# Optimization experiments

Hardware: AMD Instinct MI355X
Metric: run time of the kernel (lower is better)

Reference implementation:

```python
import jax, jax.numpy as jnp
import numpy as np

CH = 512
GROUPS = 32
EPS = 1e-6


def setup_inputs() -> dict:
    key = jax.random.key(0)
    ks = jax.random.split(key, 12)
    b, c, h, w = 4, CH, 64, 64
    std = 1.0 / np.sqrt(c)
    return {
        "x": jax.random.normal(ks[0], (b, c, h, w), dtype=jnp.float32),
        "norm_gamma": jnp.ones((c,), jnp.float32),
        "norm_beta": jnp.zeros((c,), jnp.float32),
        "wq": jax.random.normal(ks[1], (c, c), jnp.float32) * std,
        "bq": jax.random.normal(ks[2], (c,), jnp.float32) * 0.01,
        "wk": jax.random.normal(ks[3], (c, c), jnp.float32) * std,
        "bk": jax.random.normal(ks[4], (c,), jnp.float32) * 0.01,
        "wv": jax.random.normal(ks[5], (c, c), jnp.float32) * std,
        "bv": jax.random.normal(ks[6], (c,), jnp.float32) * 0.01,
        "wo": jax.random.normal(ks[7], (c, c), jnp.float32) * std,
        "bo": jax.random.normal(ks[8], (c,), jnp.float32) * 0.01,
    }


def _group_norm(x, gamma, beta):
    b, c, h, w = x.shape
    xg = x.reshape(b, GROUPS, c // GROUPS, h, w)
    mean = xg.mean(axis=(2, 3, 4), keepdims=True)
    var = xg.var(axis=(2, 3, 4), keepdims=True)
    xn = ((xg - mean) * jax.lax.rsqrt(var + EPS)).reshape(b, c, h, w)
    return xn * gamma[None, :, None, None] + beta[None, :, None, None]


def reference(x, norm_gamma, norm_beta, wq, bq, wk, bk, wv, bv, wo, bo):
    b, c, h, w = x.shape
    hn = _group_norm(x, norm_gamma, norm_beta)
    hs = hn.reshape(b, c, h * w)  # [b, c, n]
    # 1x1 convs == per-pixel matmuls over channel dim (weight[out,in])
    q = jnp.einsum('oc,bcn->bno', wq, hs) + bq  # [b, n, c]
    k = jnp.einsum('oc,bcn->bon', wk, hs) + bk[None, :, None]  # [b, c, n]
    v = jnp.einsum('oc,bcn->bno', wv, hs) + bv  # [b, n, c]
    scale = c ** (-0.5)
    attn = jax.nn.softmax(jnp.einsum('bnc,bcm->bnm', q, k) * scale, axis=-1)
    out = jnp.einsum('bnm,bmc->bnc', attn, v)  # [b, n, c]
    out = jnp.einsum('oc,bnc->bon', wo, out) + bo[None, :, None]  # [b, c, n]
    return x + out.reshape(b, c, h, w)
```

## Files before the change

kernel.cpp:

```cpp
#include <hip/hip_runtime.h>
#include <hip/hip_bf16.h>
#include <cstdint>

typedef __bf16 bf16;
typedef __bf16 bf16x8 __attribute__((ext_vector_type(8)));
typedef __bf16 bf16x4 __attribute__((ext_vector_type(4)));
typedef float f32x4 __attribute__((ext_vector_type(4)));

__device__ __forceinline__ void gld_lds16(const void* g, void* l) {
  __builtin_amdgcn_global_load_lds((const __attribute__((address_space(1))) void*)g,
                                   (__attribute__((address_space(3))) void*)l, 16, 0, 0);
}

enum { BIAS_NONE = 0, BIAS_COL = 1, BIAS_ROW = 2 };
enum { OUT_BF16 = 0, OUT_F32_RESID = 1 };

template<int BIAS_MODE, int OUT_MODE>
__global__ __launch_bounds__(256)
void gemm_bt(const bf16* __restrict__ A, long sA, int lda,
             const bf16* __restrict__ Bm, long sB, int ldb,
             void* __restrict__ Cv, long sC, int ldc,
             const float* __restrict__ bias,
             const float* __restrict__ resid, long sR,
             int K, float scale)
{
  const int bm = blockIdx.x, bn = blockIdx.y, bz = blockIdx.z;
  const char* Ab = (const char*)(A + (long)bz * sA);
  const char* Bb = (const char*)(Bm + (long)bz * sB);
  const int tid = threadIdx.x;
  const int wave = tid >> 6, lane = tid & 63;
  const int wr = wave >> 1, wc = wave & 1;

  __shared__ __attribute__((aligned(128))) char lds[32768];
  char* ldsA = lds;
  char* ldsB = lds + 16384;

  uint32_t aoff[4], boff[4];
#pragma unroll
  for (int i = 0; i < 4; ++i) {
    uint32_t ra = (uint32_t)(wr * 64 + i * 16 + (lane & 15));
    uint32_t la = ra * 128u + (uint32_t)((lane >> 4) << 4);
    aoff[i] = la ^ ((la >> 3) & 0x70u);
    uint32_t rb = (uint32_t)(wc * 64 + i * 16 + (lane & 15));
    uint32_t lb = rb * 128u + (uint32_t)((lane >> 4) << 4);
    boff[i] = lb ^ ((lb >> 3) & 0x70u);
  }

  uint32_t srow[4], sinb[4];
#pragma unroll
  for (int t = 0; t < 4; ++t) {
    uint32_t paddr = (uint32_t)(((wave * 4 + t) * 64 + lane) * 16);
    uint32_t laddr = paddr ^ ((paddr >> 3) & 0x70u);
    srow[t] = laddr >> 7;
    sinb[t] = laddr & 127u;
  }

  const long ldab = (long)lda * 2, ldbb = (long)ldb * 2;
  const long arow0 = (long)bm * 128, brow0 = (long)bn * 128;

  f32x4 acc[4][4] = {};

  const int nK = K >> 6;
  for (int kt = 0; kt < nK; ++kt) {
    const long k0b = (long)kt * 128;
#pragma unroll
    for (int t = 0; t < 4; ++t) {
      gld_lds16(Ab + (arow0 + srow[t]) * ldab + k0b + sinb[t],
                ldsA + (wave * 4 + t) * 1024);
      gld_lds16(Bb + (brow0 + srow[t]) * ldbb + k0b + sinb[t],
                ldsB + (wave * 4 + t) * 1024);
    }
    __syncthreads();
#pragma unroll
    for (int kk = 0; kk < 2; ++kk) {
      bf16x8 af[4], bfr[4];
#pragma unroll
      for (int i = 0; i < 4; ++i) {
        af[i]  = *(const bf16x8*)(ldsA + (aoff[i] ^ (kk << 6)));
        bfr[i] = *(const bf16x8*)(ldsB + (boff[i] ^ (kk << 6)));
      }
#pragma unroll
      for (int mi = 0; mi < 4; ++mi)
#pragma unroll
        for (int ni = 0; ni < 4; ++ni)
          acc[mi][ni] = __builtin_amdgcn_mfma_f32_16x16x32_bf16(af[mi], bfr[ni], acc[mi][ni], 0, 0, 0);
    }
    __syncthreads();
  }

  const int cl = lane & 15, rq = lane >> 4;
  const long row0 = (long)bm * 128 + wr * 64;
  const long col0 = (long)bn * 128 + wc * 64;

  if constexpr (OUT_MODE == OUT_BF16) {
    bf16* Co = (bf16*)Cv + (long)bz * sC;
#pragma unroll
    for (int mi = 0; mi < 4; ++mi) {
#pragma unroll
      for (int ni = 0; ni < 4; ++ni) {
        const long col = col0 + ni * 16 + cl;
        float bc = 0.f;
        if (BIAS_MODE == BIAS_COL) bc = bias[col];
#pragma unroll
        for (int j = 0; j < 4; ++j) {
          const long row = row0 + mi * 16 + rq * 4 + j;
          float v = acc[mi][ni][j] * scale + bc;
          if (BIAS_MODE == BIAS_ROW) v += bias[row];
          Co[row * ldc + col] = (bf16)v;
        }
      }
    }
  } else {
    float* Co = (float*)Cv + (long)bz * sC;
    const float* X = resid + (long)bz * sR;
#pragma unroll
    for (int mi = 0; mi < 4; ++mi) {
#pragma unroll
      for (int ni = 0; ni < 4; ++ni) {
        const long col = col0 + ni * 16 + cl;
#pragma unroll
        for (int j = 0; j < 4; ++j) {
          const long row = row0 + mi * 16 + rq * 4 + j;
          Co[row * ldc + col] = acc[mi][ni][j] + bias[row] + X[row * ldc + col];
        }
      }
    }
  }
}

__global__ __launch_bounds__(256)
void gn_stats(const float* __restrict__ x, float* __restrict__ stats)
{
  const int bg = blockIdx.x;
  const float4* px = (const float4*)(x + (long)bg * 65536);
  float s1 = 0.f, s2 = 0.f;
  for (int i = threadIdx.x; i < 16384; i += 256) {
    float4 f = px[i];
    s1 += f.x + f.y + f.z + f.w;
    s2 += f.x * f.x + f.y * f.y + f.z * f.z + f.w * f.w;
  }
#pragma unroll
  for (int d = 32; d > 0; d >>= 1) {
    s1 += __shfl_xor(s1, d, 64);
    s2 += __shfl_xor(s2, d, 64);
  }
  __shared__ float r1[4], r2[4];
  const int wave = threadIdx.x >> 6, lane = threadIdx.x & 63;
  if (lane == 0) { r1[wave] = s1; r2[wave] = s2; }
  __syncthreads();
  if (threadIdx.x == 0) {
    float t1 = r1[0] + r1[1] + r1[2] + r1[3];
    float t2 = r2[0] + r2[1] + r2[2] + r2[3];
    float mean = t1 * (1.f / 65536.f);
    float var  = t2 * (1.f / 65536.f) - mean * mean;
    stats[bg * 2]     = mean;
    stats[bg * 2 + 1] = rsqrtf(var + 1e-6f);
  }
}

__global__ __launch_bounds__(256)
void gn_apply(const float* __restrict__ x, const float* __restrict__ stats,
              const float* __restrict__ gamma, const float* __restrict__ beta,
              bf16* __restrict__ hn)
{
  const int b = blockIdx.y;
  const int n0 = blockIdx.x * 64;
  __shared__ __attribute__((aligned(16))) char lt[65536];
  const int tid = threadIdx.x;

  for (int i = 0; i < 32; ++i) {
    int f = i * 256 + tid;
    int c = f >> 4;
    int n4 = f & 15;
    float4 xv = *(const float4*)(x + (((long)b * 512 + c) * 4096) + n0 + n4 * 4);
    int g = c >> 4;
    float mean = stats[(b * 32 + g) * 2];
    float rstd = stats[(b * 32 + g) * 2 + 1];
    float ga = gamma[c], be = beta[c];
    float y[4];
    y[0] = (xv.x - mean) * rstd * ga + be;
    y[1] = (xv.y - mean) * rstd * ga + be;
    y[2] = (xv.z - mean) * rstd * ga + be;
    y[3] = (xv.w - mean) * rstd * ga + be;
    uint32_t cb = (uint32_t)(c * 2);
#pragma unroll
    for (int jj = 0; jj < 4; ++jj) {
      uint32_t nl = (uint32_t)(n4 * 4 + jj);
      uint32_t phys = nl * 1024u + (cb ^ (((nl >> 2) & 7u) << 4));
      *(bf16*)(lt + phys) = (bf16)y[jj];
    }
  }
  __syncthreads();
  for (int i = 0; i < 16; ++i) {
    int j = i * 256 + tid;
    uint32_t row = (uint32_t)(j >> 6);
    uint32_t m = (uint32_t)(j & 63);
    uint32_t phys = row * 1024u + ((m * 16u) ^ (((row >> 2) & 7u) << 4));
    uint4 val = *(const uint4*)(lt + phys);
    *(uint4*)((char*)(hn + ((long)b * 4096 + n0 + row) * 512) + m * 16) = val;
  }
}

__global__ __launch_bounds__(256)
void f32_to_bf16_k(const float* __restrict__ src, bf16* __restrict__ dst, int n4)
{
  int i = blockIdx.x * 256 + threadIdx.x;
  if (i < n4) {
    float4 f = ((const float4*)src)[i];
    bf16x4 o;
    o[0] = (bf16)f.x; o[1] = (bf16)f.y; o[2] = (bf16)f.z; o[3] = (bf16)f.w;
    ((bf16x4*)dst)[i] = o;
  }
}

__global__ __launch_bounds__(256)
void softmax_rows(bf16* __restrict__ S)
{
  const long row = (long)blockIdx.x * 4 + (threadIdx.x >> 6);
  const int lane = threadIdx.x & 63;
  bf16* p = S + row * 4096;
  float v[64];
#pragma unroll
  for (int i = 0; i < 8; ++i) {
    bf16x8 c = *(const bf16x8*)(p + (i * 64 + lane) * 8);
#pragma unroll
    for (int j = 0; j < 8; ++j) v[i * 8 + j] = (float)c[j];
  }
  float m = -3.0e38f;
#pragma unroll
  for (int i = 0; i < 64; ++i) m = fmaxf(m, v[i]);
#pragma unroll
  for (int d = 32; d > 0; d >>= 1) m = fmaxf(m, __shfl_xor(m, d, 64));
  float s = 0.f;
#pragma unroll
  for (int i = 0; i < 64; ++i) { v[i] = __expf(v[i] - m); s += v[i]; }
#pragma unroll
  for (int d = 32; d > 0; d >>= 1) s += __shfl_xor(s, d, 64);
  const float r = 1.f / s;
#pragma unroll
  for (int i = 0; i < 8; ++i) {
    bf16x8 c;
#pragma unroll
    for (int j = 0; j < 8; ++j) c[j] = (bf16)(v[i * 8 + j] * r);
    *(bf16x8*)(p + (i * 64 + lane) * 8) = c;
  }
}

extern "C" void kernel_launch(void* const* d_in, const int* in_sizes, int n_in,
                              void* d_out, int out_size, void* d_ws, size_t ws_size,
                              hipStream_t stream)
{
  const float* x     = (const float*)d_in[0];
  const float* gamma = (const float*)d_in[1];
  const float* beta  = (const float*)d_in[2];
  const float* wq = (const float*)d_in[3];
  const float* bq = (const float*)d_in[4];
  const float* wk = (const float*)d_in[5];
  const float* bk = (const float*)d_in[6];
  const float* wv = (const float*)d_in[7];
  const float* bv = (const float*)d_in[8];
  const float* wo = (const float*)d_in[9];
  const float* bo = (const float*)d_in[10];
  float* out = (float*)d_out;

  char* ws = (char*)d_ws;
  bf16* hn  = (bf16*)(ws + 0);
  bf16* q   = (bf16*)(ws + 16777216);
  bf16* k   = (bf16*)(ws + 33554432);
  bf16* v   = (bf16*)(ws + 50331648);
  bf16* O   = (bf16*)(ws + 67108864);
  bf16* wqb = (bf16*)(ws + 83886080);
  bf16* wkb = (bf16*)(ws + 84410368);
  bf16* wvb = (bf16*)(ws + 84934656);
  bf16* wob = (bf16*)(ws + 85458944);
  float* stats = (float*)(ws + 85983232);
  bf16* S   = (bf16*)(ws + 85984256);

  const long sBC = 2097152;
  const long sS1 = 16777216;
  const float scale = 0.044194173824159216f;

  f32_to_bf16_k<<<256, 256, 0, stream>>>(wq, wqb, 65536);
  f32_to_bf16_k<<<256, 256, 0, stream>>>(wk, wkb, 65536);
  f32_to_bf16_k<<<256, 256, 0, stream>>>(wv, wvb, 65536);
  f32_to_bf16_k<<<256, 256, 0, stream>>>(wo, wob, 65536);
  gn_stats<<<128, 256, 0, stream>>>(x, stats);
  gn_apply<<<dim3(64, 4), 256, 0, stream>>>(x, stats, gamma, beta, hn);

  gemm_bt<BIAS_COL, OUT_BF16><<<dim3(32, 4, 4), 256, 0, stream>>>(
      hn, sBC, 512, wqb, 0, 512, q, sBC, 512, bq, nullptr, 0, 512, 1.f);
  gemm_bt<BIAS_COL, OUT_BF16><<<dim3(32, 4, 4), 256, 0, stream>>>(
      hn, sBC, 512, wkb, 0, 512, k, sBC, 512, bk, nullptr, 0, 512, 1.f);
  gemm_bt<BIAS_ROW, OUT_BF16><<<dim3(4, 32, 4), 256, 0, stream>>>(
      wvb, 0, 512, hn, sBC, 512, v, sBC, 4096, bv, nullptr, 0, 512, 1.f);

  const bool tier1 = ws_size >= (size_t)220201984;
  if (tier1) {
    gemm_bt<BIAS_NONE, OUT_BF16><<<dim3(32, 32, 4), 256, 0, stream>>>(
        q, sBC, 512, k, sBC, 512, S, sS1, 4096, nullptr, nullptr, 0, 512, scale);
    softmax_rows<<<4096, 256, 0, stream>>>(S);
    gemm_bt<BIAS_NONE, OUT_BF16><<<dim3(32, 4, 4), 256, 0, stream>>>(
        S, sS1, 4096, v, sBC, 4096, O, sBC, 512, nullptr, nullptr, 0, 4096, 1.f);
  } else {
    for (int b = 0; b < 4; ++b) {
      gemm_bt<BIAS_NONE, OUT_BF16><<<dim3(32, 32, 1), 256, 0, stream>>>(
          q + b * sBC, 0, 512, k + b * sBC, 0, 512, S, 0, 4096, nullptr, nullptr, 0, 512, scale);
      softmax_rows<<<1024, 256, 0, stream>>>(S);
      gemm_bt<BIAS_NONE, OUT_BF16><<<dim3(32, 4, 1), 256, 0, stream>>>(
          S, 0, 4096, v + b * sBC, 0, 4096, O + b * sBC, 0, 512, nullptr, nullptr, 0, 4096, 1.f);
    }
  }

  gemm_bt<BIAS_ROW, OUT_F32_RESID><<<dim3(4, 32, 4), 256, 0, stream>>>(
      wob, 0, 512, O, sBC, 512, out, sBC, 4096, bo, x, sBC, 512, 1.f);
}
```

Before: 307.9 us.

## Replace materialized QK/softmax/PV with fused flash attention kernel

```diff
diff --git a/kernel.cpp b/kernel.cpp
--- a/kernel.cpp
+++ b/kernel.cpp
@@ -20,7 +20,7 @@
 void gemm_bt(const bf16* __restrict__ A, long sA, int lda,
              const bf16* __restrict__ Bm, long sB, int ldb,
              void* __restrict__ Cv, long sC, int ldc,
-             const float* __restrict__ bias,
+             const float* __restrict__ bias, float bscale,
              const float* __restrict__ resid, long sR,
              int K, float scale)
 {
@@ -100,12 +100,12 @@
       for (int ni = 0; ni < 4; ++ni) {
         const long col = col0 + ni * 16 + cl;
         float bc = 0.f;
-        if (BIAS_MODE == BIAS_COL) bc = bias[col];
+        if (BIAS_MODE == BIAS_COL) bc = bias[col] * bscale;
 #pragma unroll
         for (int j = 0; j < 4; ++j) {
           const long row = row0 + mi * 16 + rq * 4 + j;
           float v = acc[mi][ni][j] * scale + bc;
-          if (BIAS_MODE == BIAS_ROW) v += bias[row];
+          if (BIAS_MODE == BIAS_ROW) v += bias[row] * bscale;
           Co[row * ldc + col] = (bf16)v;
         }
       }
@@ -121,11 +121,214 @@
 #pragma unroll
         for (int j = 0; j < 4; ++j) {
           const long row = row0 + mi * 16 + rq * 4 + j;
-          Co[row * ldc + col] = acc[mi][ni][j] + bias[row] + X[row * ldc + col];
+          Co[row * ldc + col] = acc[mi][ni][j] + bias[row] * bscale + X[row * ldc + col];
         }
       }
     }
   }
+}
+
+#define FA_LDS_SIZE 149504
+
+__global__ __launch_bounds__(512, 2)
+void flash_attn(const bf16* __restrict__ Qg, const bf16* __restrict__ Kg,
+                const bf16* __restrict__ Vg, bf16* __restrict__ Og)
+{
+  extern __shared__ char lds[];
+  char* ldsQ = lds;
+  char* buf0 = lds + 65536;
+  char* buf1 = lds + 98304;
+  char* ldsP = lds + 131072;
+  float* pred = (float*)(lds + 147456);
+
+  const int bid = blockIdx.x;
+  const int b  = (bid & 7) >> 1;
+  const int rb = ((bid >> 3) << 1) | (bid & 1);
+  const int n0 = rb * 64;
+  const int tid = threadIdx.x;
+  const int wave = tid >> 6, lane = tid & 63;
+  const int wr = wave >> 2, wc = wave & 3;
+  const int lg = lane >> 4, l15 = lane & 15;
+
+  const char* Qb = (const char*)(Qg + ((long)b * 4096 + n0) * 512);
+  const char* Kb = (const char*)(Kg + (long)b * 4096 * 512);
+  const char* Vb = (const char*)(Vg + (long)b * 512 * 4096);
+
+  uint32_t q_goff[8], k_goff[4], v_goff[4];
+#pragma unroll
+  for (int it = 0; it < 8; ++it) {
+    uint32_t s = it * 512 + tid;
+    uint32_t row = s >> 6, off = (s & 63) * 16;
+    q_goff[it] = row * 1024 + (off ^ ((row & 7) << 4));
+  }
+#pragma unroll
+  for (int it = 0; it < 4; ++it) {
+    uint32_t s = it * 512 + tid;
+    uint32_t row = s >> 4, off = (s & 15) * 16;
+    k_goff[it] = row * 1024 + (off ^ ((row & 7) << 4));
+  }
+#pragma unroll
+  for (int it = 0; it < 4; ++it) {
+    uint32_t s = it * 512 + tid;
+    uint32_t d = s >> 2, off = (s & 3) * 16;
+    v_goff[it] = d * 8192 + (off ^ (((d >> 1) & 3) << 4));
+  }
+  const uint32_t dst0 = (uint32_t)tid * 16;
+
+  uint32_t qb_[2], qs_[2], pb_[2], ps_[2], kb_[2], ks_[2], vb_[8], vs_[8];
+#pragma unroll
+  for (int mi = 0; mi < 2; ++mi) {
+    uint32_t r = wr * 32 + mi * 16 + l15;
+    qb_[mi] = r * 1024; qs_[mi] = (r & 7) << 4;
+    pb_[mi] = r * 256;  ps_[mi] = (r & 7) << 4;
+  }
+#pragma unroll
+  for (int ni = 0; ni < 2; ++ni) {
+    uint32_t r = wc * 32 + ni * 16 + l15;
+    kb_[ni] = r * 256; ks_[ni] = (r & 7) << 4;
+  }
+#pragma unroll
+  for (int ni = 0; ni < 8; ++ni) {
+    uint32_t d = wc * 128 + ni * 16 + l15;
+    vb_[ni] = d * 64; vs_[ni] = ((d >> 1) & 3) << 4;
+  }
+
+  f32x4 acc_o[2][8] = {};
+  f32x4 acc_s[2][2] = {};
+  float m_run[2][4], l_run[2][4];
+#pragma unroll
+  for (int mi = 0; mi < 2; ++mi)
+#pragma unroll
+    for (int j = 0; j < 4; ++j) { m_run[mi][j] = -3.0e38f; l_run[mi][j] = 0.f; }
+
+  auto stage_k = [&](char* buf, long kv0, int dc) {
+    const char* src = Kb + kv0 * 1024 + dc * 256;
+#pragma unroll
+    for (int it = 0; it < 4; ++it)
+      gld_lds16(src + k_goff[it], buf + it * 8192 + dst0);
+  };
+  auto stage_v = [&](char* buf, long kvcol) {
+    const char* src = Vb + kvcol * 2;
+#pragma unroll
+    for (int it = 0; it < 4; ++it)
+      gld_lds16(src + v_goff[it], buf + it * 8192 + dst0);
+  };
+  auto qk_phase = [&](const char* kb, int dc) {
+#pragma unroll
+    for (int kk = 0; kk < 4; ++kk) {
+      bf16x8 a[2], bb[2];
+#pragma unroll
+      for (int mi = 0; mi < 2; ++mi)
+        a[mi] = *(const bf16x8*)(ldsQ + qb_[mi] + ((uint32_t)(dc * 256 + kk * 64 + lg * 16) ^ qs_[mi]));
+#pragma unroll
+      for (int ni = 0; ni < 2; ++ni)
+        bb[ni] = *(const bf16x8*)(kb + kb_[ni] + ((uint32_t)(kk * 64 + lg * 16) ^ ks_[ni]));
+#pragma unroll
+      for (int mi = 0; mi < 2; ++mi)
+#pragma unroll
+        for (int ni = 0; ni < 2; ++ni)
+          acc_s[mi][ni] = __builtin_amdgcn_mfma_f32_16x16x32_bf16(a[mi], bb[ni], acc_s[mi][ni], 0, 0, 0);
+    }
+  };
+  auto pv_phase = [&](const char* vbuf, int s) {
+    bf16x8 a[2];
+#pragma unroll
+    for (int mi = 0; mi < 2; ++mi)
+      a[mi] = *(const bf16x8*)(ldsP + pb_[mi] + ((uint32_t)(s * 64 + lg * 16) ^ ps_[mi]));
+#pragma unroll
+    for (int ni = 0; ni < 8; ++ni) {
+      bf16x8 bb = *(const bf16x8*)(vbuf + vb_[ni] + ((uint32_t)(lg * 16) ^ vs_[ni]));
+#pragma unroll
+      for (int mi = 0; mi < 2; ++mi)
+        acc_o[mi][ni] = __builtin_amdgcn_mfma_f32_16x16x32_bf16(a[mi], bb, acc_o[mi][ni], 0, 0, 0);
+    }
+  };
+
+#pragma unroll
+  for (int it = 0; it < 8; ++it)
+    gld_lds16(Qb + q_goff[it], ldsQ + it * 8192 + dst0);
+  stage_k(buf0, 0, 0);
+  __syncthreads();
+
+  for (int t = 0; t < 32; ++t) {
+    const long kv0 = (long)t * 128;
+    stage_k(buf1, kv0, 1);  qk_phase(buf0, 0); __syncthreads();
+    stage_k(buf0, kv0, 2);  qk_phase(buf1, 1); __syncthreads();
+    stage_k(buf1, kv0, 3);  qk_phase(buf0, 2); __syncthreads();
+    stage_v(buf0, kv0);     qk_phase(buf1, 3); __syncthreads();
+
+    float tmx[2][4];
+#pragma unroll
+    for (int mi = 0; mi < 2; ++mi)
+#pragma unroll
+      for (int j = 0; j < 4; ++j) {
+        float tv = fmaxf(acc_s[mi][0][j], acc_s[mi][1][j]);
+#pragma unroll
+        for (int d = 1; d < 16; d <<= 1) tv = fmaxf(tv, __shfl_xor(tv, d, 64));
+        tmx[mi][j] = tv;
+      }
+    if (l15 == 0) {
+#pragma unroll
+      for (int mi = 0; mi < 2; ++mi)
+#pragma unroll
+        for (int j = 0; j < 4; ++j)
+          pred[(wr * 32 + mi * 16 + lg * 4 + j) * 4 + wc] = tmx[mi][j];
+    }
+    __syncthreads();
+
+#pragma unroll
+    for (int mi = 0; mi < 2; ++mi)
+#pragma unroll
+      for (int j = 0; j < 4; ++j) {
+        const int row = wr * 32 + mi * 16 + lg * 4 + j;
+        float4 pm = *(const float4*)&pred[row * 4];
+        float tm = fmaxf(fmaxf(pm.x, pm.y), fmaxf(pm.z, pm.w));
+        float mnew = fmaxf(m_run[mi][j], tm);
+        float alpha = __expf(m_run[mi][j] - mnew);
+        m_run[mi][j] = mnew;
+        l_run[mi][j] *= alpha;
+#pragma unroll
+        for (int ni = 0; ni < 8; ++ni) acc_o[mi][ni][j] *= alpha;
+#pragma unroll
+        for (int ni = 0; ni < 2; ++ni) {
+          float p = __expf(acc_s[mi][ni][j] - mnew);
+          l_run[mi][j] += p;
+          const int col = wc * 32 + ni * 16 + l15;
+          *(bf16*)(ldsP + row * 256 + (((uint32_t)(col * 2)) ^ ((row & 7) << 4))) = (bf16)p;
+          acc_s[mi][ni][j] = 0.f;
+        }
+      }
+    __syncthreads();
+
+    stage_v(buf1, kv0 + 32);  pv_phase(buf0, 0); __syncthreads();
+    stage_v(buf0, kv0 + 64);  pv_phase(buf1, 1); __syncthreads();
+    stage_v(buf1, kv0 + 96);  pv_phase(buf0, 2); __syncthreads();
+    if (t < 31) stage_k(buf0, kv0 + 128, 0);
+    pv_phase(buf1, 3); __syncthreads();
+  }
+
+#pragma unroll
+  for (int mi = 0; mi < 2; ++mi)
+#pragma unroll
+    for (int j = 0; j < 4; ++j) {
+      float l = l_run[mi][j];
+#pragma unroll
+      for (int d = 1; d < 16; d <<= 1) l += __shfl_xor(l, d, 64);
+      if (l15 == 0) pred[(wr * 32 + mi * 16 + lg * 4 + j) * 4 + wc] = l;
+    }
+  __syncthreads();
+  bf16* Ob = Og + ((long)b * 4096 + n0) * 512;
+#pragma unroll
+  for (int mi = 0; mi < 2; ++mi)
+#pragma unroll
+    for (int j = 0; j < 4; ++j) {
+      const int row = wr * 32 + mi * 16 + lg * 4 + j;
+      float4 s4 = *(const float4*)&pred[row * 4];
+      float r = 1.f / (s4.x + s4.y + s4.z + s4.w);
+#pragma unroll
+      for (int ni = 0; ni < 8; ++ni)
+        Ob[(long)row * 512 + wc * 128 + ni * 16 + l15] = (bf16)(acc_o[mi][ni][j] * r);
+    }
 }
 
 __global__ __launch_bounds__(256)
@@ -213,39 +416,6 @@
   }
 }
 
-__global__ __launch_bounds__(256)
-void softmax_rows(bf16* __restrict__ S)
-{
-  const long row = (long)blockIdx.x * 4 + (threadIdx.x >> 6);
-  const int lane = threadIdx.x & 63;
-  bf16* p = S + row * 4096;
-  float v[64];
-#pragma unroll
-  for (int i = 0; i < 8; ++i) {
-    bf16x8 c = *(const bf16x8*)(p + (i * 64 + lane) * 8);
-#pragma unroll
-    for (int j = 0; j < 8; ++j) v[i * 8 + j] = (float)c[j];
-  }
-  float m = -3.0e38f;
-#pragma unroll
-  for (int i = 0; i < 64; ++i) m = fmaxf(m, v[i]);
-#pragma unroll
-  for (int d = 32; d > 0; d >>= 1) m = fmaxf(m, __shfl_xor(m, d, 64));
-  float s = 0.f;
-#pragma unroll
-  for (int i = 0; i < 64; ++i) { v[i] = __expf(v[i] - m); s += v[i]; }
-#pragma unroll
-  for (int d = 32; d > 0; d >>= 1) s += __shfl_xor(s, d, 64);
-  const float r = 1.f / s;
-#pragma unroll
-  for (int i = 0; i < 8; ++i) {
-    bf16x8 c;
-#pragma unroll
-    for (int j = 0; j < 8; ++j) c[j] = (bf16)(v[i * 8 + j] * r);
-    *(bf16x8*)(p + (i * 64 + lane) * 8) = c;
-  }
-}
-
 extern "C" void kernel_launch(void* const* d_in, const int* in_sizes, int n_in,
                               void* d_out, int out_size, void* d_ws, size_t ws_size,
                               hipStream_t stream)
@@ -274,11 +444,12 @@
   bf16* wvb = (bf16*)(ws + 84934656);
   bf16* wob = (bf16*)(ws + 85458944);
   float* stats = (float*)(ws + 85983232);
-  bf16* S   = (bf16*)(ws + 85984256);
 
   const long sBC = 2097152;
-  const long sS1 = 16777216;
   const float scale = 0.044194173824159216f;
+
+  hipFuncSetAttribute(reinterpret_cast<const void*>(flash_attn),
+                      hipFuncAttributeMaxDynamicSharedMemorySize, FA_LDS_SIZE);
 
   f32_to_bf16_k<<<256, 256, 0, stream>>>(wq, wqb, 65536);
   f32_to_bf16_k<<<256, 256, 0, stream>>>(wk, wkb, 65536);
@@ -288,29 +459,14 @@
   gn_apply<<<dim3(64, 4), 256, 0, stream>>>(x, stats, gamma, beta, hn);
 
   gemm_bt<BIAS_COL, OUT_BF16><<<dim3(32, 4, 4), 256, 0, stream>>>(
-      hn, sBC, 512, wqb, 0, 512, q, sBC, 512, bq, nullptr, 0, 512, 1.f);
+      hn, sBC, 512, wqb, 0, 512, q, sBC, 512, bq, scale, nullptr, 0, 512, scale);
   gemm_bt<BIAS_COL, OUT_BF16><<<dim3(32, 4, 4), 256, 0, stream>>>(
-      hn, sBC, 512, wkb, 0, 512, k, sBC, 512, bk, nullptr, 0, 512, 1.f);
+      hn, sBC, 512, wkb, 0, 512, k, sBC, 512, bk, 1.f, nullptr, 0, 512, 1.f);
   gemm_bt<BIAS_ROW, OUT_BF16><<<dim3(4, 32, 4), 256, 0, stream>>>(
-      wvb, 0, 512, hn, sBC, 512, v, sBC, 4096, bv, nullptr, 0, 512, 1.f);
-
-  const bool tier1 = ws_size >= (size_t)220201984;
-  if (tier1) {
-    gemm_bt<BIAS_NONE, OUT_BF16><<<dim3(32, 32, 4), 256, 0, stream>>>(
-        q, sBC, 512, k, sBC, 512, S, sS1, 4096, nullptr, nullptr, 0, 512, scale);
-    softmax_rows<<<4096, 256, 0, stream>>>(S);
-    gemm_bt<BIAS_NONE, OUT_BF16><<<dim3(32, 4, 4), 256, 0, stream>>>(
-        S, sS1, 4096, v, sBC, 4096, O, sBC, 512, nullptr, nullptr, 0, 4096, 1.f);
-  } else {
-    for (int b = 0; b < 4; ++b) {
-      gemm_bt<BIAS_NONE, OUT_BF16><<<dim3(32, 32, 1), 256, 0, stream>>>(
-          q + b * sBC, 0, 512, k + b * sBC, 0, 512, S, 0, 4096, nullptr, nullptr, 0, 512, scale);
-      softmax_rows<<<1024, 256, 0, stream>>>(S);
-      gemm_bt<BIAS_NONE, OUT_BF16><<<dim3(32, 4, 1), 256, 0, stream>>>(
-          S, 0, 4096, v + b * sBC, 0, 4096, O + b * sBC, 0, 512, nullptr, nullptr, 0, 4096, 1.f);
-    }
-  }
+      wvb, 0, 512, hn, sBC, 512, v, sBC, 4096, bv, 1.f, nullptr, 0, 512, 1.f);
+
+  flash_attn<<<256, 512, FA_LDS_SIZE, stream>>>(q, k, v, O);
 
   gemm_bt<BIAS_ROW, OUT_F32_RESID><<<dim3(4, 32, 4), 256, 0, stream>>>(
-      wob, 0, 512, O, sBC, 512, out, sBC, 4096, bo, x, sBC, 512, 1.f);
-}
+      wob, 0, 512, O, sBC, 512, out, sBC, 4096, bo, 1.f, x, sBC, 512, 1.f);
+}
```

New measurement: 402.6 us. 1.31x slower.

## Add double-buffered 8-wave GEMM for QK^T and PV, fold softmax scale into Q

Applied to the files above, without the earlier changes.

```diff
diff --git a/kernel.cpp b/kernel.cpp
--- a/kernel.cpp
+++ b/kernel.cpp
@@ -10,6 +10,163 @@
 __device__ __forceinline__ void gld_lds16(const void* g, void* l) {
   __builtin_amdgcn_global_load_lds((const __attribute__((address_space(1))) void*)g,
                                    (__attribute__((address_space(3))) void*)l, 16, 0, 0);
+}
+__device__ __forceinline__ void bar() { asm volatile("s_barrier" ::: "memory"); }
+template<int N> __device__ __forceinline__ void vmwaitc() {
+  asm volatile("s_waitcnt vmcnt(%0)" :: "i"(N) : "memory");
+}
+
+template<int MI>
+__global__ __launch_bounds__(512, 2)
+void gemm8p(const bf16* __restrict__ A, long sA, int lda,
+            const bf16* __restrict__ Bm, long sB, int ldb,
+            bf16* __restrict__ C, long sC, int ldc,
+            int K, float scale)
+{
+  constexpr int WNW = MI / 2;
+  constexpr int BN = WNW * 64;
+  constexpr int BLOADS = BN / 128;
+  constexpr int NQ0 = 4 + BLOADS;
+  constexpr int NQ3 = 4 + 2 * BLOADS;
+  constexpr int NQ3E = 2 + BLOADS;
+  constexpr int HR = MI * 8;
+  constexpr int HRL = (MI == 8) ? 6 : 5;
+  constexpr int ATILE = 32768;
+  constexpr int BTILE = BN * 128;
+  constexpr int MIH = MI / 2;
+
+  extern __shared__ char lds[];
+  char* ldsA = lds;
+  char* ldsB = lds + 2 * ATILE;
+
+  const int bm = blockIdx.x, bn = blockIdx.y, bz = blockIdx.z;
+  const int tid = threadIdx.x, wave = tid >> 6, lane = tid & 63;
+  const int wr = wave / WNW, wc = wave % WNW;
+  const int lg = lane >> 4, l15 = lane & 15;
+  const long ldab = (long)lda * 2, ldbb = (long)ldb * 2;
+  const char* Ab = (const char*)(A + (long)bz * sA) + (long)bm * 256 * ldab;
+  const char* Bb = (const char*)(Bm + (long)bz * sB) + (long)bn * BN * ldbb;
+  const int T = K >> 6;
+
+  uint32_t aR0[2], aIn[2];
+#pragma unroll
+  for (int j = 0; j < 2; ++j) {
+    uint32_t s = j * 512 + tid, r = s >> 3;
+    aIn[j] = (s & 7) * 16;
+    aR0[j] = (r >> HRL) * (MI * 16) + (r & (HR - 1));
+  }
+  uint32_t bR0[BLOADS], bIn[BLOADS];
+#pragma unroll
+  for (int j = 0; j < BLOADS; ++j) {
+    uint32_t s = j * 512 + tid, r = s >> 3;
+    bIn[j] = (s & 7) * 16;
+    bR0[j] = (r >> 5) * 64 + (r & 31);
+  }
+
+  const uint32_t swz = (uint32_t)(l15 & 7) << 4;
+  uint32_t aBase[2][MIH], bBase[2][2];
+#pragma unroll
+  for (int mh = 0; mh < 2; ++mh)
+#pragma unroll
+    for (int mi2 = 0; mi2 < MIH; ++mi2) {
+      uint32_t row = wr * (MI * 16) + mh * HR + mi2 * 16 + l15;
+      aBase[mh][mi2] = row * 128 + ((uint32_t)(lg * 16) ^ swz);
+    }
+#pragma unroll
+  for (int nh = 0; nh < 2; ++nh)
+#pragma unroll
+    for (int ni2 = 0; ni2 < 2; ++ni2) {
+      uint32_t row = wc * 64 + nh * 32 + ni2 * 16 + l15;
+      bBase[nh][ni2] = row * 128 + ((uint32_t)(lg * 16) ^ swz);
+    }
+
+  f32x4 acc[MI][4] = {};
+  bf16x8 aF[MIH][2], bF[2][2];
+
+  auto stageA = [&](int h, int tt) {
+#pragma unroll
+    for (int j = 0; j < 2; ++j) {
+      uint32_t R = aR0[j] + (uint32_t)h * HR;
+      gld_lds16(Ab + (long)R * ldab + (long)tt * 128 + (aIn[j] ^ ((aR0[j] & 7) << 4)),
+                ldsA + (uint32_t)(tt & 1) * ATILE + R * 128 + aIn[j]);
+    }
+  };
+  auto stageB = [&](int h, int tt) {
+#pragma unroll
+    for (int j = 0; j < BLOADS; ++j) {
+      uint32_t R = bR0[j] + (uint32_t)h * 32;
+      gld_lds16(Bb + (long)R * ldbb + (long)tt * 128 + (bIn[j] ^ ((bR0[j] & 7) << 4)),
+                ldsB + (uint32_t)(tt & 1) * BTILE + R * 128 + bIn[j]);
+    }
+  };
+
+  stageA(0, 0); stageB(0, 0); stageA(1, 0); stageB(1, 0);
+  if (T > 1) { stageA(0, 1); stageB(0, 1); }
+  if (T > 1) vmwaitc<NQ3>(); else vmwaitc<0>();
+  bar();
+
+  for (int t = 0; t < T; ++t) {
+    const uint32_t bufA = (uint32_t)(t & 1) * ATILE;
+    const uint32_t bufB = (uint32_t)(t & 1) * BTILE;
+
+#pragma unroll
+    for (int q = 0; q < 4; ++q) {
+      const int mh = q >> 1, nh = q & 1;
+      if (nh == 0) {
+#pragma unroll
+        for (int mi2 = 0; mi2 < MIH; ++mi2)
+#pragma unroll
+          for (int kk = 0; kk < 2; ++kk)
+            aF[mi2][kk] = *(const bf16x8*)(ldsA + ((bufA + aBase[mh][mi2]) ^ (uint32_t)(kk << 6)));
+      }
+#pragma unroll
+      for (int ni2 = 0; ni2 < 2; ++ni2)
+#pragma unroll
+        for (int kk = 0; kk < 2; ++kk)
+          bF[ni2][kk] = *(const bf16x8*)(ldsB + ((bufB + bBase[nh][ni2]) ^ (uint32_t)(kk << 6)));
+
+      if (q == 0)      { if (t + 1 < T) stageA(1, t + 1); }
+      else if (q == 1) { if (t + 1 < T) stageB(1, t + 1); }
+      else if (q == 2) { if (t + 2 < T) stageA(0, t + 2); }
+      else             { if (t + 2 < T) stageB(0, t + 2); }
+
+      bar();
+      __builtin_amdgcn_s_setprio(1);
+#pragma unroll
+      for (int mi2 = 0; mi2 < MIH; ++mi2)
+#pragma unroll
+        for (int ni2 = 0; ni2 < 2; ++ni2)
+#pragma unroll
+          for (int kk = 0; kk < 2; ++kk)
+            acc[mh * MIH + mi2][nh * 2 + ni2] =
+              __builtin_amdgcn_mfma_f32_16x16x32_bf16(aF[mi2][kk], bF[ni2][kk],
+                                                      acc[mh * MIH + mi2][nh * 2 + ni2], 0, 0, 0);
+      __builtin_amdgcn_s_setprio(0);
+
+      if (q == 0) {
+        if (t + 1 < T) vmwaitc<NQ0>(); else vmwaitc<0>();
+      } else if (q == 3) {
+        if (t + 1 < T) { if (t + 2 < T) vmwaitc<NQ3>(); else vmwaitc<NQ3E>(); }
+      }
+      bar();
+    }
+  }
+
+  bf16* Co = C + (long)bz * sC;
+  const int cl = l15, rq = lg;
+  const long row0 = (long)bm * 256 + wr * (MI * 16);
+  const long col0 = (long)bn * BN + wc * 64;
+#pragma unroll
+  for (int mi = 0; mi < MI; ++mi)
+#pragma unroll
+    for (int ni = 0; ni < 4; ++ni) {
+      const long col = col0 + ni * 16 + cl;
+#pragma unroll
+      for (int j = 0; j < 4; ++j) {
+        const long row = row0 + mi * 16 + rq * 4 + j;
+        Co[row * ldc + col] = (bf16)(acc[mi][ni][j] * scale);
+      }
+    }
 }
 
 enum { BIAS_NONE = 0, BIAS_COL = 1, BIAS_ROW = 2 };
@@ -20,7 +177,7 @@
 void gemm_bt(const bf16* __restrict__ A, long sA, int lda,
              const bf16* __restrict__ Bm, long sB, int ldb,
              void* __restrict__ Cv, long sC, int ldc,
-             const float* __restrict__ bias,
+             const float* __restrict__ bias, float bscale,
              const float* __restrict__ resid, long sR,
              int K, float scale)
 {
@@ -45,7 +202,6 @@
     uint32_t lb = rb * 128u + (uint32_t)((lane >> 4) << 4);
     boff[i] = lb ^ ((lb >> 3) & 0x70u);
   }
-
   uint32_t srow[4], sinb[4];
 #pragma unroll
   for (int t = 0; t < 4; ++t) {
@@ -57,18 +213,14 @@
 
   const long ldab = (long)lda * 2, ldbb = (long)ldb * 2;
   const long arow0 = (long)bm * 128, brow0 = (long)bn * 128;
-
   f32x4 acc[4][4] = {};
-
   const int nK = K >> 6;
   for (int kt = 0; kt < nK; ++kt) {
     const long k0b = (long)kt * 128;
 #pragma unroll
     for (int t = 0; t < 4; ++t) {
-      gld_lds16(Ab + (arow0 + srow[t]) * ldab + k0b + sinb[t],
-                ldsA + (wave * 4 + t) * 1024);
-      gld_lds16(Bb + (brow0 + srow[t]) * ldbb + k0b + sinb[t],
-                ldsB + (wave * 4 + t) * 1024);
+      gld_lds16(Ab + (arow0 + srow[t]) * ldab + k0b + sinb[t], ldsA + (wave * 4 + t) * 1024);
+      gld_lds16(Bb + (brow0 + srow[t]) * ldbb + k0b + sinb[t], ldsB + (wave * 4 + t) * 1024);
     }
     __syncthreads();
 #pragma unroll
@@ -91,40 +243,37 @@
   const int cl = lane & 15, rq = lane >> 4;
   const long row0 = (long)bm * 128 + wr * 64;
   const long col0 = (long)bn * 128 + wc * 64;
-
   if constexpr (OUT_MODE == OUT_BF16) {
     bf16* Co = (bf16*)Cv + (long)bz * sC;
 #pragma unroll
-    for (int mi = 0; mi < 4; ++mi) {
+    for (int mi = 0; mi < 4; ++mi)
 #pragma unroll
       for (int ni = 0; ni < 4; ++ni) {
         const long col = col0 + ni * 16 + cl;
         float bc = 0.f;
-        if (BIAS_MODE == BIAS_COL) bc = bias[col];
+        if (BIAS_MODE == BIAS_COL) bc = bias[col] * bscale;
 #pragma unroll
         for (int j = 0; j < 4; ++j) {
           const long row = row0 + mi * 16 + rq * 4 + j;
           float v = acc[mi][ni][j] * scale + bc;
-          if (BIAS_MODE == BIAS_ROW) v += bias[row];
+          if (BIAS_MODE == BIAS_ROW) v += bias[row] * bscale;
           Co[row * ldc + col] = (bf16)v;
         }
       }
-    }
   } else {
     float* Co = (float*)Cv + (long)bz * sC;
     const float* X = resid + (long)bz * sR;
 #pragma unroll
-    for (int mi = 0; mi < 4; ++mi) {
+    for (int mi = 0; mi < 4; ++mi)
 #pragma unroll
       for (int ni = 0; ni < 4; ++ni) {
         const long col = col0 + ni * 16 + cl;
 #pragma unroll
         for (int j = 0; j < 4; ++j) {
           const long row = row0 + mi * 16 + rq * 4 + j;
-          Co[row * ldc + col] = acc[mi][ni][j] + bias[row] + X[row * ldc + col];
+          Co[row * ldc + col] = acc[mi][ni][j] + bias[row] * bscale + X[row * ldc + col];
         }
       }
-    }
   }
 }
 
@@ -167,7 +316,6 @@
   const int n0 = blockIdx.x * 64;
   __shared__ __attribute__((aligned(16))) char lt[65536];
   const int tid = threadIdx.x;
-
   for (int i = 0; i < 32; ++i) {
     int f = i * 256 + tid;
     int c = f >> 4;
@@ -280,6 +428,13 @@
   const long sS1 = 16777216;
   const float scale = 0.044194173824159216f;
 
+  const int LDS_S  = 131072;
+  const int LDS_PV = 98304;
+  hipFuncSetAttribute(reinterpret_cast<const void*>(gemm8p<8>),
+                      hipFuncAttributeMaxDynamicSharedMemorySize, LDS_S);
+  hipFuncSetAttribute(reinterpret_cast<const void*>(gemm8p<4>),
+                      hipFuncAttributeMaxDynamicSharedMemorySize, LDS_PV);
+
   f32_to_bf16_k<<<256, 256, 0, stream>>>(wq, wqb, 65536);
   f32_to_bf16_k<<<256, 256, 0, stream>>>(wk, wkb, 65536);
   f32_to_bf16_k<<<256, 256, 0, stream>>>(wv, wvb, 65536);
@@ -288,29 +443,29 @@
   gn_apply<<<dim3(64, 4), 256, 0, stream>>>(x, stats, gamma, beta, hn);
 
   gemm_bt<BIAS_COL, OUT_BF16><<<dim3(32, 4, 4), 256, 0, stream>>>(
-      hn, sBC, 512, wqb, 0, 512, q, sBC, 512, bq, nullptr, 0, 512, 1.f);
+      hn, sBC, 512, wqb, 0, 512, q, sBC, 512, bq, scale, nullptr, 0, 512, scale);
   gemm_bt<BIAS_COL, OUT_BF16><<<dim3(32, 4, 4), 256, 0, stream>>>(
-      hn, sBC, 512, wkb, 0, 512, k, sBC, 512, bk, nullptr, 0, 512, 1.f);
+      hn, sBC, 512, wkb, 0, 512, k, sBC, 512, bk, 1.f, nullptr, 0, 512, 1.f);
   gemm_bt<BIAS_ROW, OUT_BF16><<<dim3(4, 32, 4), 256, 0, stream>>>(
-      wvb, 0, 512, hn, sBC, 512, v, sBC, 4096, bv, nullptr, 0, 512, 1.f);
+      wvb, 0, 512, hn, sBC, 512, v, sBC, 4096, bv, 1.f, nullptr, 0, 512, 1.f);
 
   const bool tier1 = ws_size >= (size_t)220201984;
   if (tier1) {
-    gemm_bt<BIAS_NONE, OUT_BF16><<<dim3(32, 32, 4), 256, 0, stream>>>(
-        q, sBC, 512, k, sBC, 512, S, sS1, 4096, nullptr, nullptr, 0, 512, scale);
+    gemm8p<8><<<dim3(16, 16, 4), 512, LDS_S, stream>>>(
+        q, sBC, 512, k, sBC, 512, S, sS1, 4096, 512, 1.f);
     softmax_rows<<<4096, 256, 0, stream>>>(S);
-    gemm_bt<BIAS_NONE, OUT_BF16><<<dim3(32, 4, 4), 256, 0, stream>>>(
-        S, sS1, 4096, v, sBC, 4096, O, sBC, 512, nullptr, nullptr, 0, 4096, 1.f);
+    gemm8p<4><<<dim3(16, 4, 4), 512, LDS_PV, stream>>>(
+        S, sS1, 4096, v, sBC, 4096, O, sBC, 512, 4096, 1.f);
   } else {
     for (int b = 0; b < 4; ++b) {
-      gemm_bt<BIAS_NONE, OUT_BF16><<<dim3(32, 32, 1), 256, 0, stream>>>(
-          q + b * sBC, 0, 512, k + b * sBC, 0, 512, S, 0, 4096, nullptr, nullptr, 0, 512, scale);
+      gemm8p<8><<<dim3(16, 16, 1), 512, LDS_S, stream>>>(
+          q + b * sBC, 0, 512, k + b * sBC, 0, 512, S, 0, 4096, 512, 1.f);
       softmax_rows<<<1024, 256, 0, stream>>>(S);
-      gemm_bt<BIAS_NONE, OUT_BF16><<<dim3(32, 4, 1), 256, 0, stream>>>(
-          S, 0, 4096, v + b * sBC, 0, 4096, O + b * sBC, 0, 512, nullptr, nullptr, 0, 4096, 1.f);
+      gemm8p<4><<<dim3(16, 4, 1), 512, LDS_PV, stream>>>(
+          S, 0, 4096, v + b * sBC, 0, 4096, O + b * sBC, 0, 512, 4096, 1.f);
     }
   }
 
   gemm_bt<BIAS_ROW, OUT_F32_RESID><<<dim3(4, 32, 4), 256, 0, stream>>>(
-      wob, 0, 512, O, sBC, 512, out, sBC, 4096, bo, x, sBC, 512, 1.f);
-}
+      wob, 0, 512, O, sBC, 512, out, sBC, 4096, bo, 1.f, x, sBC, 512, 1.f);
+}
```

After: 322.5 us. 1.05x slower.

## Fuse softmax stats into QK^T epilogue and normalize in PV GEMM prologue

Applied to the files above, without the earlier changes.

```diff
diff --git a/kernel.cpp b/kernel.cpp
--- a/kernel.cpp
+++ b/kernel.cpp
@@ -12,16 +12,17 @@
                                    (__attribute__((address_space(3))) void*)l, 16, 0, 0);
 }
 
-enum { BIAS_NONE = 0, BIAS_COL = 1, BIAS_ROW = 2 };
-enum { OUT_BF16 = 0, OUT_F32_RESID = 1 };
+enum { BIAS_NONE = 0, BIAS_COL = 1, BIAS_ROW = 2, BIAS_QK = 3 };
+enum { OUT_BF16 = 0, OUT_F32_RESID = 1, OUT_SM = 2 };
 
 template<int BIAS_MODE, int OUT_MODE>
 __global__ __launch_bounds__(256)
 void gemm_bt(const bf16* __restrict__ A, long sA, int lda,
              const bf16* __restrict__ Bm, long sB, int ldb,
              void* __restrict__ Cv, long sC, int ldc,
-             const float* __restrict__ bias,
+             const float* __restrict__ bias, const float* __restrict__ bias2,
              const float* __restrict__ resid, long sR,
+             float* __restrict__ mp, float* __restrict__ lp,
              int K, float scale)
 {
   const int bm = blockIdx.x, bn = blockIdx.y, bz = blockIdx.z;
@@ -45,7 +46,6 @@
     uint32_t lb = rb * 128u + (uint32_t)((lane >> 4) << 4);
     boff[i] = lb ^ ((lb >> 3) & 0x70u);
   }
-
   uint32_t srow[4], sinb[4];
 #pragma unroll
   for (int t = 0; t < 4; ++t) {
@@ -57,18 +57,14 @@
 
   const long ldab = (long)lda * 2, ldbb = (long)ldb * 2;
   const long arow0 = (long)bm * 128, brow0 = (long)bn * 128;
-
   f32x4 acc[4][4] = {};
-
   const int nK = K >> 6;
   for (int kt = 0; kt < nK; ++kt) {
     const long k0b = (long)kt * 128;
 #pragma unroll
     for (int t = 0; t < 4; ++t) {
-      gld_lds16(Ab + (arow0 + srow[t]) * ldab + k0b + sinb[t],
-                ldsA + (wave * 4 + t) * 1024);
-      gld_lds16(Bb + (brow0 + srow[t]) * ldbb + k0b + sinb[t],
-                ldsB + (wave * 4 + t) * 1024);
+      gld_lds16(Ab + (arow0 + srow[t]) * ldab + k0b + sinb[t], ldsA + (wave * 4 + t) * 1024);
+      gld_lds16(Bb + (brow0 + srow[t]) * ldbb + k0b + sinb[t], ldsB + (wave * 4 + t) * 1024);
     }
     __syncthreads();
 #pragma unroll
@@ -92,29 +88,11 @@
   const long row0 = (long)bm * 128 + wr * 64;
   const long col0 = (long)bn * 128 + wc * 64;
 
-  if constexpr (OUT_MODE == OUT_BF16) {
-    bf16* Co = (bf16*)Cv + (long)bz * sC;
-#pragma unroll
-    for (int mi = 0; mi < 4; ++mi) {
-#pragma unroll
-      for (int ni = 0; ni < 4; ++ni) {
-        const long col = col0 + ni * 16 + cl;
-        float bc = 0.f;
-        if (BIAS_MODE == BIAS_COL) bc = bias[col];
-#pragma unroll
-        for (int j = 0; j < 4; ++j) {
-          const long row = row0 + mi * 16 + rq * 4 + j;
-          float v = acc[mi][ni][j] * scale + bc;
-          if (BIAS_MODE == BIAS_ROW) v += bias[row];
-          Co[row * ldc + col] = (bf16)v;
-        }
-      }
-    }
-  } else {
+  if constexpr (OUT_MODE == OUT_F32_RESID) {
     float* Co = (float*)Cv + (long)bz * sC;
     const float* X = resid + (long)bz * sR;
 #pragma unroll
-    for (int mi = 0; mi < 4; ++mi) {
+    for (int mi = 0; mi < 4; ++mi)
 #pragma unroll
       for (int ni = 0; ni < 4; ++ni) {
         const long col = col0 + ni * 16 + cl;
@@ -124,8 +102,186 @@
           Co[row * ldc + col] = acc[mi][ni][j] + bias[row] + X[row * ldc + col];
         }
       }
-    }
-  }
+  } else if constexpr (BIAS_MODE == BIAS_QK) {
+    const bool isq = (col0 < 512);
+    bf16* base = (bf16*)Cv + (long)bz * sC + (isq ? 0 : sR);
+    const long csub = isq ? 0 : 512;
+#pragma unroll
+    for (int mi = 0; mi < 4; ++mi)
+#pragma unroll
+      for (int ni = 0; ni < 4; ++ni) {
+        const long col = col0 + ni * 16 + cl;
+        const float bc = isq ? bias[col] * scale : bias2[col - 512];
+        const float vs = isq ? scale : 1.f;
+#pragma unroll
+        for (int j = 0; j < 4; ++j) {
+          const long row = row0 + mi * 16 + rq * 4 + j;
+          base[row * ldc + (col - csub)] = (bf16)(acc[mi][ni][j] * vs + bc);
+        }
+      }
+  } else {
+    bf16* Co = (bf16*)Cv + (long)bz * sC;
+#pragma unroll
+    for (int mi = 0; mi < 4; ++mi)
+#pragma unroll
+      for (int ni = 0; ni < 4; ++ni) {
+        const long col = col0 + ni * 16 + cl;
+        float bc = 0.f;
+        if (BIAS_MODE == BIAS_COL) bc = bias[col] * scale;
+#pragma unroll
+        for (int j = 0; j < 4; ++j) {
+          const long row = row0 + mi * 16 + rq * 4 + j;
+          float v = acc[mi][ni][j] * (BIAS_MODE == BIAS_COL ? scale : 1.f) + bc;
+          if (BIAS_MODE == BIAS_ROW) v += bias[row];
+          Co[row * ldc + col] = (bf16)v;
+        }
+      }
+    if constexpr (OUT_MODE == OUT_SM) {
+      float m64[4][4], e64[4][4];
+#pragma unroll
+      for (int mi = 0; mi < 4; ++mi)
+#pragma unroll
+        for (int j = 0; j < 4; ++j) {
+          float mm = fmaxf(fmaxf(acc[mi][0][j], acc[mi][1][j]),
+                           fmaxf(acc[mi][2][j], acc[mi][3][j]));
+          mm = fmaxf(mm, __shfl_xor(mm, 1, 64));
+          mm = fmaxf(mm, __shfl_xor(mm, 2, 64));
+          mm = fmaxf(mm, __shfl_xor(mm, 4, 64));
+          mm = fmaxf(mm, __shfl_xor(mm, 8, 64));
+          float ee = __expf(acc[mi][0][j] - mm) + __expf(acc[mi][1][j] - mm)
+                   + __expf(acc[mi][2][j] - mm) + __expf(acc[mi][3][j] - mm);
+          ee += __shfl_xor(ee, 1, 64);
+          ee += __shfl_xor(ee, 2, 64);
+          ee += __shfl_xor(ee, 4, 64);
+          ee += __shfl_xor(ee, 8, 64);
+          m64[mi][j] = mm; e64[mi][j] = ee;
+        }
+      if (cl == 0) {
+        const long stripe = (long)bn * 2 + wc;
+        const long rowbase = (long)bz * 4096 + row0;
+#pragma unroll
+        for (int mi = 0; mi < 4; ++mi)
+#pragma unroll
+          for (int j = 0; j < 4; ++j) {
+            const long idx = (rowbase + mi * 16 + rq * 4 + j) * 64 + stripe;
+            mp[idx] = m64[mi][j];
+            lp[idx] = e64[mi][j];
+          }
+      }
+    }
+  }
+}
+
+__global__ __launch_bounds__(256)
+void sm_combine(const float* __restrict__ mp, const float* __restrict__ lp,
+                float2* __restrict__ rs)
+{
+  const long row = (long)blockIdx.x * 4 + (threadIdx.x >> 6);
+  const int lane = threadIdx.x & 63;
+  float m = mp[row * 64 + lane];
+  float l = lp[row * 64 + lane];
+  float M = m;
+#pragma unroll
+  for (int d = 32; d > 0; d >>= 1) M = fmaxf(M, __shfl_xor(M, d, 64));
+  float t = __expf(m - M) * l;
+#pragma unroll
+  for (int d = 32; d > 0; d >>= 1) t += __shfl_xor(t, d, 64);
+  if (lane == 0) rs[row] = make_float2(M, 1.f / t);
+}
+
+__global__ __launch_bounds__(256)
+void gemm_pv(const bf16* __restrict__ S, long sA,
+             const bf16* __restrict__ Vm, long sB,
+             bf16* __restrict__ O, long sC,
+             const float2* __restrict__ rstat, long sRS,
+             int K)
+{
+  const int bm = blockIdx.x, bn = blockIdx.y, bz = blockIdx.z;
+  const char* Ab = (const char*)(S + (long)bz * sA);
+  const char* Bb = (const char*)(Vm + (long)bz * sB);
+  const float2* rs = rstat + (long)bz * sRS;
+  const int tid = threadIdx.x;
+  const int wave = tid >> 6, lane = tid & 63;
+  const int wr = wave >> 1, wc = wave & 1;
+
+  __shared__ __attribute__((aligned(128))) char lds[32768];
+  char* ldsA = lds;
+  char* ldsB = lds + 16384;
+
+  uint32_t aoff[4], boff[4];
+#pragma unroll
+  for (int i = 0; i < 4; ++i) {
+    uint32_t ra = (uint32_t)(wr * 64 + i * 16 + (lane & 15));
+    uint32_t la = ra * 128u + (uint32_t)((lane >> 4) << 4);
+    aoff[i] = la ^ ((la >> 3) & 0x70u);
+    uint32_t rb = (uint32_t)(wc * 64 + i * 16 + (lane & 15));
+    uint32_t lb = rb * 128u + (uint32_t)((lane >> 4) << 4);
+    boff[i] = lb ^ ((lb >> 3) & 0x70u);
+  }
+  uint32_t srow[4], sinb[4];
+#pragma unroll
+  for (int t = 0; t < 4; ++t) {
+    uint32_t paddr = (uint32_t)(((wave * 4 + t) * 64 + lane) * 16);
+    uint32_t laddr = paddr ^ ((paddr >> 3) & 0x70u);
+    srow[t] = laddr >> 7;
+    sinb[t] = laddr & 127u;
+  }
+  const uint32_t ar = (uint32_t)(tid >> 3);
+  const uint32_t ab0 = (uint32_t)((tid & 7) * 16);
+
+  const long ldab = 8192, ldbb = 8192;
+  const long arow0 = (long)bm * 128, brow0 = (long)bn * 128;
+  f32x4 acc[4][4] = {};
+  const int nK = K >> 6;
+  for (int kt = 0; kt < nK; ++kt) {
+    const long k0b = (long)kt * 128;
+#pragma unroll
+    for (int t = 0; t < 4; ++t)
+      gld_lds16(Bb + (brow0 + srow[t]) * ldbb + k0b + sinb[t], ldsB + (wave * 4 + t) * 1024);
+#pragma unroll
+    for (int p = 0; p < 4; ++p) {
+      const uint32_t r = p * 32 + ar;
+      bf16x8 sv = *(const bf16x8*)(Ab + (arow0 + r) * ldab + k0b + ab0);
+      const float2 st = rs[arow0 + r];
+      bf16x8 pv;
+#pragma unroll
+      for (int j = 0; j < 8; ++j)
+        pv[j] = (bf16)(__expf((float)sv[j] - st.x) * st.y);
+      *(bf16x8*)(ldsA + r * 128 + (ab0 ^ ((r & 7) << 4))) = pv;
+    }
+    __syncthreads();
+#pragma unroll
+    for (int kk = 0; kk < 2; ++kk) {
+      bf16x8 af[4], bfr[4];
+#pragma unroll
+      for (int i = 0; i < 4; ++i) {
+        af[i]  = *(const bf16x8*)(ldsA + (aoff[i] ^ (kk << 6)));
+        bfr[i] = *(const bf16x8*)(ldsB + (boff[i] ^ (kk << 6)));
+      }
+#pragma unroll
+      for (int mi = 0; mi < 4; ++mi)
+#pragma unroll
+        for (int ni = 0; ni < 4; ++ni)
+          acc[mi][ni] = __builtin_amdgcn_mfma_f32_16x16x32_bf16(af[mi], bfr[ni], acc[mi][ni], 0, 0, 0);
+    }
+    __syncthreads();
+  }
+
+  const int cl = lane & 15, rq = lane >> 4;
+  const long row0 = (long)bm * 128 + wr * 64;
+  const long col0 = (long)bn * 128 + wc * 64;
+  bf16* Co = O + (long)bz * sC;
+#pragma unroll
+  for (int mi = 0; mi < 4; ++mi)
+#pragma unroll
+    for (int ni = 0; ni < 4; ++ni) {
+      const long col = col0 + ni * 16 + cl;
+#pragma unroll
+      for (int j = 0; j < 4; ++j) {
+        const long row = row0 + mi * 16 + rq * 4 + j;
+        Co[row * 512 + col] = (bf16)acc[mi][ni][j];
+      }
+    }
 }
 
 __global__ __launch_bounds__(256)
@@ -167,7 +323,6 @@
   const int n0 = blockIdx.x * 64;
   __shared__ __attribute__((aligned(16))) char lt[65536];
   const int tid = threadIdx.x;
-
   for (int i = 0; i < 32; ++i) {
     int f = i * 256 + tid;
     int c = f >> 4;
@@ -202,48 +357,17 @@
 }
 
 __global__ __launch_bounds__(256)
-void f32_to_bf16_k(const float* __restrict__ src, bf16* __restrict__ dst, int n4)
-{
-  int i = blockIdx.x * 256 + threadIdx.x;
-  if (i < n4) {
-    float4 f = ((const float4*)src)[i];
-    bf16x4 o;
-    o[0] = (bf16)f.x; o[1] = (bf16)f.y; o[2] = (bf16)f.z; o[3] = (bf16)f.w;
-    ((bf16x4*)dst)[i] = o;
-  }
-}
-
-__global__ __launch_bounds__(256)
-void softmax_rows(bf16* __restrict__ S)
-{
-  const long row = (long)blockIdx.x * 4 + (threadIdx.x >> 6);
-  const int lane = threadIdx.x & 63;
-  bf16* p = S + row * 4096;
-  float v[64];
-#pragma unroll
-  for (int i = 0; i < 8; ++i) {
-    bf16x8 c = *(const bf16x8*)(p + (i * 64 + lane) * 8);
-#pragma unroll
-    for (int j = 0; j < 8; ++j) v[i * 8 + j] = (float)c[j];
-  }
-  float m = -3.0e38f;
-#pragma unroll
-  for (int i = 0; i < 64; ++i) m = fmaxf(m, v[i]);
-#pragma unroll
-  for (int d = 32; d > 0; d >>= 1) m = fmaxf(m, __shfl_xor(m, d, 64));
-  float s = 0.f;
-#pragma unroll
-  for (int i = 0; i < 64; ++i) { v[i] = __expf(v[i] - m); s += v[i]; }
-#pragma unroll
-  for (int d = 32; d > 0; d >>= 1) s += __shfl_xor(s, d, 64);
-  const float r = 1.f / s;
-#pragma unroll
-  for (int i = 0; i < 8; ++i) {
-    bf16x8 c;
-#pragma unroll
-    for (int j = 0; j < 8; ++j) c[j] = (bf16)(v[i * 8 + j] * r);
-    *(bf16x8*)(p + (i * 64 + lane) * 8) = c;
-  }
+void conv_w4(const float* __restrict__ w0, const float* __restrict__ w1,
+             const float* __restrict__ w2, const float* __restrict__ w3,
+             bf16* __restrict__ dst)
+{
+  const int z = blockIdx.y;
+  const float* src = (z == 0) ? w0 : (z == 1) ? w1 : (z == 2) ? w2 : w3;
+  const int i = blockIdx.x * 256 + threadIdx.x;
+  float4 f = ((const float4*)src)[i];
+  bf16x4 o;
+  o[0] = (bf16)f.x; o[1] = (bf16)f.y; o[2] = (bf16)f.z; o[3] = (bf16)f.w;
+  ((bf16x4*)(dst))[(long)z * 65536 + i] = o;
 }
 
 extern "C" void kernel_launch(void* const* d_in, const int* in_sizes, int n_in,
@@ -270,47 +394,50 @@
   bf16* v   = (bf16*)(ws + 50331648);
   bf16* O   = (bf16*)(ws + 67108864);
   bf16* wqb = (bf16*)(ws + 83886080);
-  bf16* wkb = (bf16*)(ws + 84410368);
   bf16* wvb = (bf16*)(ws + 84934656);
   bf16* wob = (bf16*)(ws + 85458944);
-  float* stats = (float*)(ws + 85983232);
-  bf16* S   = (bf16*)(ws + 85984256);
+  float* gstats = (float*)(ws + 85983232);
+  float* mpart  = (float*)(ws + 85984256);
+  float* lpart  = (float*)(ws + 90178560);
+  float2* rstat = (float2*)(ws + 94372864);
+  bf16* S   = (bf16*)(ws + 94503936);
 
   const long sBC = 2097152;
   const long sS1 = 16777216;
+  const long K_OFS = 8388608;
   const float scale = 0.044194173824159216f;
 
-  f32_to_bf16_k<<<256, 256, 0, stream>>>(wq, wqb, 65536);
-  f32_to_bf16_k<<<256, 256, 0, stream>>>(wk, wkb, 65536);
-  f32_to_bf16_k<<<256, 256, 0, stream>>>(wv, wvb, 65536);
-  f32_to_bf16_k<<<256, 256, 0, stream>>>(wo, wob, 65536);
-  gn_stats<<<128, 256, 0, stream>>>(x, stats);
-  gn_apply<<<dim3(64, 4), 256, 0, stream>>>(x, stats, gamma, beta, hn);
-
-  gemm_bt<BIAS_COL, OUT_BF16><<<dim3(32, 4, 4), 256, 0, stream>>>(
-      hn, sBC, 512, wqb, 0, 512, q, sBC, 512, bq, nullptr, 0, 512, 1.f);
-  gemm_bt<BIAS_COL, OUT_BF16><<<dim3(32, 4, 4), 256, 0, stream>>>(
-      hn, sBC, 512, wkb, 0, 512, k, sBC, 512, bk, nullptr, 0, 512, 1.f);
+  conv_w4<<<dim3(256, 4), 256, 0, stream>>>(wq, wk, wv, wo, wqb);
+  gn_stats<<<128, 256, 0, stream>>>(x, gstats);
+  gn_apply<<<dim3(64, 4), 256, 0, stream>>>(x, gstats, gamma, beta, hn);
+
+  gemm_bt<BIAS_QK, OUT_BF16><<<dim3(32, 8, 4), 256, 0, stream>>>(
+      hn, sBC, 512, wqb, 0, 512, q, sBC, 512,
+      bq, bk, nullptr, K_OFS, nullptr, nullptr, 512, scale);
   gemm_bt<BIAS_ROW, OUT_BF16><<<dim3(4, 32, 4), 256, 0, stream>>>(
-      wvb, 0, 512, hn, sBC, 512, v, sBC, 4096, bv, nullptr, 0, 512, 1.f);
-
-  const bool tier1 = ws_size >= (size_t)220201984;
+      wvb, 0, 512, hn, sBC, 512, v, sBC, 4096,
+      bv, nullptr, nullptr, 0, nullptr, nullptr, 512, 1.f);
+
+  const bool tier1 = ws_size >= (size_t)228721664;
   if (tier1) {
-    gemm_bt<BIAS_NONE, OUT_BF16><<<dim3(32, 32, 4), 256, 0, stream>>>(
-        q, sBC, 512, k, sBC, 512, S, sS1, 4096, nullptr, nullptr, 0, 512, scale);
-    softmax_rows<<<4096, 256, 0, stream>>>(S);
-    gemm_bt<BIAS_NONE, OUT_BF16><<<dim3(32, 4, 4), 256, 0, stream>>>(
-        S, sS1, 4096, v, sBC, 4096, O, sBC, 512, nullptr, nullptr, 0, 4096, 1.f);
+    gemm_bt<BIAS_NONE, OUT_SM><<<dim3(32, 32, 4), 256, 0, stream>>>(
+        q, sBC, 512, k, sBC, 512, S, sS1, 4096,
+        nullptr, nullptr, nullptr, 0, mpart, lpart, 512, 1.f);
+    sm_combine<<<4096, 256, 0, stream>>>(mpart, lpart, rstat);
+    gemm_pv<<<dim3(32, 4, 4), 256, 0, stream>>>(
+        S, sS1, v, sBC, O, sBC, rstat, 4096, 4096);
   } else {
     for (int b = 0; b < 4; ++b) {
-      gemm_bt<BIAS_NONE, OUT_BF16><<<dim3(32, 32, 1), 256, 0, stream>>>(
-          q + b * sBC, 0, 512, k + b * sBC, 0, 512, S, 0, 4096, nullptr, nullptr, 0, 512, scale);
-      softmax_rows<<<1024, 256, 0, stream>>>(S);
-      gemm_bt<BIAS_NONE, OUT_BF16><<<dim3(32, 4, 1), 256, 0, stream>>>(
-          S, 0, 4096, v + b * sBC, 0, 4096, O + b * sBC, 0, 512, nullptr, nullptr, 0, 4096, 1.f);
+      gemm_bt<BIAS_NONE, OUT_SM><<<dim3(32, 32, 1), 256, 0, stream>>>(
+          q + b * sBC, 0, 512, k + b * sBC, 0, 512, S, 0, 4096,
+          nullptr, nullptr, nullptr, 0, mpart, lpart, 512, 1.f);
+      sm_combine<<<1024, 256, 0, stream>>>(mpart, lpart, rstat);
+      gemm_pv<<<dim3(32, 4, 1), 256, 0, stream>>>(
+          S, 0, v + b * sBC, 0, O + b * sBC, 0, rstat, 0, 4096);
     }
   }
 
   gemm_bt<BIAS_ROW, OUT_F32_RESID><<<dim3(4, 32, 4), 256, 0, stream>>>(
-      wob, 0, 512, O, sBC, 512, out, sBC, 4096, bo, x, sBC, 512, 1.f);
-}
+      wob, 0, 512, O, sBC, 512, out, sBC, 4096,
+      bo, nullptr, x, sBC, nullptr, nullptr, 512, 1.f);
+}
```

Result: slower. 362.0 us (+17.6%).
